# Optimization experiments

Measured on AMD Instinct MI355X. Metric: run time of the kernel, lower is better.

Reference implementation:

```python
import jax, jax.numpy as jnp
import numpy as np

VISUAL_WEIGHT = 0.01

def setup_inputs() -> dict:
    key = jax.random.key(0)
    ks = jax.random.split(key, 10)
    h = w = 96
    inp = {
        'feat_src': jax.random.normal(ks[0], (1, 256, h, w), jnp.float32),
        'feat_ref': jax.random.normal(ks[1], (1, 256, h, w), jnp.float32),
        'landmarks_src': jax.random.normal(ks[2], (1, 136, h, w), jnp.float32),
        'landmarks_ref': jax.random.normal(ks[3], (1, 136, h, w), jnp.float32),
        'mask_src': jax.random.randint(ks[4], (1, 1, h, w), 0, 3, jnp.int32),
        'mask_ref': jax.random.randint(ks[5], (1, 1, h, w), 0, 3, jnp.int32),
        'conv1_w': jax.random.normal(ks[6], (256,), jnp.float32) * 0.05,
        'conv1_b': jax.random.normal(ks[7], (1,), jnp.float32) * 0.05,
        'conv2_w': jax.random.normal(ks[8], (256,), jnp.float32) * 0.05,
        'conv2_b': jax.random.normal(ks[9], (1,), jnp.float32) * 0.05,
    }
    return inp

def reference(feat_src, feat_ref, landmarks_src, landmarks_ref, mask_src, mask_ref,
              conv1_w, conv1_b, conv2_w, conv2_b):
    b, c, h, w = feat_src.shape  # b == 1 assumed by original code
    hw = h * w
    ck = c + 136
    # 1x1 convs (256 -> 1): einsum over channel
    beta = jnp.einsum('bchw,c->bhw', feat_ref, conv1_w) + conv1_b[:, None, None]  # (1,h,w)
    gama = jnp.einsum('bchw,c->bhw', feat_ref, conv2_w) + conv2_b[:, None, None]
    # concat visual features with landmark heatmaps, then RAW reshape (as in torch)
    src = jnp.concatenate([VISUAL_WEIGHT * feat_src, landmarks_src], axis=1)  # (1,392,h,w)
    ref = jnp.concatenate([VISUAL_WEIGHT * feat_ref, landmarks_ref], axis=1)
    feat_lm_src = jnp.reshape(src, (hw, ck))   # raw reshape, faithful to torch
    feat_lm_ref = jnp.reshape(ref, (ck, hw))
    # element-wise mask equality -> (hw,) vector, broadcast over columns of A
    M = (jnp.reshape(mask_src, (hw,)) == jnp.reshape(mask_ref, (hw,))).astype(feat_src.dtype)
    A = feat_lm_src @ feat_lm_ref            # (hw, hw)
    A = jax.nn.softmax(A, axis=0)
    A = A * M                                 # broadcast on last dim, same as torch
    beta_hat = jnp.reshape(A @ jnp.reshape(beta, (hw, 1)), (1, h, w))
    gama_hat = jnp.reshape(A @ jnp.reshape(gama, (hw, 1)), (1, h, w))
    # gama_hat.expand((1,1,h,w)) * feat_src + beta_hat
    feat_src_trans = gama_hat[None] * feat_src + beta_hat[None]
    return feat_src_trans
```

## Files before the change

### kernel.cpp

```cpp
#include <hip/hip_runtime.h>

#define HW    9216
#define CK    392
#define NVIS  2359296
#define KP    672
#define NKT   21
#define NRB   144
#define MAXN  3584
#define NB_N  28
#define PSRC_BLOCKS 3024

typedef __bf16 bf16_t;
typedef __bf16 bf16x8 __attribute__((ext_vector_type(8)));
typedef __bf16 bf16x4v __attribute__((ext_vector_type(4)));
typedef unsigned short ushort8v __attribute__((ext_vector_type(8)));
typedef float  f32x4  __attribute__((ext_vector_type(4)));

typedef __attribute__((address_space(1))) void void_g;
typedef __attribute__((address_space(3))) void void_l;

static __device__ __forceinline__ void gload16(const void* g, void* l) {
  __builtin_amdgcn_global_load_lds((const void_g*)g, (void_l*)l, 16, 0, 0);
}

__global__ __launch_bounds__(256) void fused_prep(
    const float* __restrict__ feat_src, const float* __restrict__ lm_src,
    const float* __restrict__ fr, const int* __restrict__ ms,
    const int* __restrict__ mr, const float* __restrict__ w1,
    const float* __restrict__ b1, const float* __restrict__ w2,
    const float* __restrict__ b2,
    bf16_t* __restrict__ Sp, int* __restrict__ sel,
    float* __restrict__ wbs, float* __restrict__ wgs, int* __restrict__ cnt)
{
  __shared__ float r1[4][64], r2[4][64];
  __shared__ int sb[4], st[4];
  int bid = blockIdx.x, t = threadIdx.x;

  if (bid < PSRC_BLOCKS) {
    int tid = bid * 256 + t;
    int i = tid / 84, kc = tid - i * 84;
    int ko = kc * 8;
    int j0 = 0; bool lo = false, zero = false;
    if (kc < 49)       j0 = ko;
    else if (kc < 66)  j0 = ko - 136;
    else if (kc < 83) { j0 = ko - 272; lo = true; }
    else               zero = true;
    bf16x8 pk = {};
    if (!zero) {
      int idx0 = i * CK + j0;
      const float* src = (idx0 < NVIS) ? (feat_src + idx0) : (lm_src + (idx0 - NVIS));
      float sc = (idx0 < NVIS) ? 0.01f : 1.f;
      float4 v0 = *reinterpret_cast<const float4*>(src);
      float4 v1 = *reinterpret_cast<const float4*>(src + 4);
      float x[8] = {v0.x, v0.y, v0.z, v0.w, v1.x, v1.y, v1.z, v1.w};
      #pragma unroll
      for (int e = 0; e < 8; ++e) {
        float xv = sc * x[e];
        bf16_t h = (bf16_t)xv;
        pk[e] = lo ? (bf16_t)(xv - (float)h) : h;
      }
    }
    *reinterpret_cast<bf16x8*>(Sp + (long)tid * 8) = pk;
  } else {
    int b = bid - PSRC_BLOCKS;
    int qi = t & 63, cg = t >> 6, lane = t & 63, wid = t >> 6;
    int q0 = b * 64;
    float a1 = 0.f, a2 = 0.f;
    #pragma unroll 4
    for (int c = cg * 64; c < cg * 64 + 64; ++c) {
      float v = fr[(long)c * HW + q0 + qi];
      a1 += v * w1[c]; a2 += v * w2[c];
    }
    r1[cg][qi] = a1; r2[cg][qi] = a2;
    int cb = 0, ct = 0;
    for (int q = t; q < HW; q += 256) {
      bool f = (ms[q] == mr[q]);
      ct += f ? 1 : 0;
      cb += (f && q < q0) ? 1 : 0;
    }
    #pragma unroll
    for (int d = 1; d < 64; d <<= 1) {
      cb += __shfl_xor(cb, d);
      ct += __shfl_xor(ct, d);
    }
    if (lane == 0) { sb[wid] = cb; st[wid] = ct; }
    __syncthreads();
    int base = sb[0] + sb[1] + sb[2] + sb[3];
    if (t == 0 && b == 0) cnt[0] = st[0] + st[1] + st[2] + st[3];
    if (wid == 0) {
      int q = q0 + lane;
      bool flag = (ms[q] == mr[q]);
      unsigned long long mk = __ballot(flag);
      int pos = __popcll(mk & ((1ull << lane) - 1ull));
      if (flag) {
        int idx = base + pos;
        sel[idx] = q;
        wbs[idx] = r1[0][lane] + r1[1][lane] + r1[2][lane] + r1[3][lane] + b1[0];
        wgs[idx] = r2[0][lane] + r2[1][lane] + r2[2][lane] + r2[3][lane] + b2[0];
      }
    }
  }
}

__global__ __launch_bounds__(256) void prep_ref(
    const float* __restrict__ feat_ref, const float* __restrict__ lm_ref,
    const int* __restrict__ sel, const int* __restrict__ cnt,
    bf16_t* __restrict__ Rp)
{
  int nsel = cnt[0];
  int n128 = (nsel + 127) & ~127;
  int qt = blockIdx.y;
  if (qt * 32 >= n128) return;
  __shared__ bf16_t tile[32][33];
  int x = threadIdx.x & 31, y = threadIdx.x >> 5;
  int kt = blockIdx.x;
  int n = qt * 32 + x;
  int q = (n < nsel) ? sel[n] : -1;
  #pragma unroll
  for (int ry = 0; ry < 4; ++ry) {
    int kl = y + ry * 8;
    int k = kt * 32 + kl;
    int j = -1; bool lo = false;
    if (k < 392)      j = k;
    else if (k < 528) { j = k - 136; lo = true; }
    else if (k < 664) j = k - 272;
    bf16_t v = (bf16_t)0.f;
    if (j >= 0 && q >= 0) {
      int idx = j * HW + q;
      float xv = (idx < NVIS) ? 0.01f * feat_ref[idx] : lm_ref[idx - NVIS];
      bf16_t h = (bf16_t)xv;
      v = lo ? (bf16_t)(xv - (float)h) : h;
    }
    tile[kl][x] = v;
  }
  __syncthreads();
  #pragma unroll
  for (int ry = 0; ry < 4; ++ry) {
    int ql = y + ry * 8;
    int k = kt * 32 + x;
    Rp[(long)(qt * 32 + ql) * KP + k] = tile[x][ql];
  }
}

__global__ __launch_bounds__(256, 2) void gemm_e(
    const bf16_t* __restrict__ Sp, const bf16_t* __restrict__ Rp,
    const int* __restrict__ cnt, bf16_t* __restrict__ E, float* __restrict__ pd)
{
  const int bm = blockIdx.x, bn = blockIdx.y;
  if (bn * 128 >= ((cnt[0] + 127) & ~127)) return;
  __shared__ __align__(16) bf16_t As[128 * 32];
  __shared__ __align__(16) bf16_t Bs[128 * 32];
  const int t = threadIdx.x, w = t >> 6, lane = t & 63;
  const int wr = w >> 1, wc = w & 1;
  f32x4 acc[4][4] = {};

  const int chs = ((lane & 3) ^ ((lane >> 3) & 3)) * 8;
  const bf16_t* sA = Sp + (long)(bm * 128 + w * 32 + (lane >> 2)) * KP + chs;
  const bf16_t* sB = Rp + (long)(bn * 128 + w * 32 + (lane >> 2)) * KP + chs;
  bf16_t* lA = As + w * 1024;
  bf16_t* lB = Bs + w * 1024;
  const int sub = lane >> 4, r16 = lane & 15;
  const int swz = (sub ^ ((r16 >> 1) & 3)) * 8;
  const int aoff = (wr * 64 + r16) * 32 + swz;
  const int boff = (wc * 64 + r16) * 32 + swz;

  for (int kt = 0; kt < NKT; ++kt) {
    gload16(sA, lA);
    gload16(sA + 16 * KP, lA + 512);
    gload16(sB, lB);
    gload16(sB + 16 * KP, lB + 512);
    sA += 32; sB += 32;
    __syncthreads();
    bf16x8 a[4], b[4];
    #pragma unroll
    for (int m = 0; m < 4; ++m)
      a[m] = *reinterpret_cast<const bf16x8*>(As + aoff + m * 512);
    #pragma unroll
    for (int n = 0; n < 4; ++n)
      b[n] = *reinterpret_cast<const bf16x8*>(Bs + boff + n * 512);
    #pragma unroll
    for (int m = 0; m < 4; ++m)
      #pragma unroll
      for (int n = 0; n < 4; ++n)
        acc[m][n] = __builtin_amdgcn_mfma_f32_16x16x32_bf16(a[m], b[n], acc[m][n], 0, 0, 0);
    __syncthreads();
  }

  #pragma unroll
  for (int m = 0; m < 4; ++m)
    #pragma unroll
    for (int n = 0; n < 4; ++n)
      #pragma unroll
      for (int r = 0; r < 4; ++r)
        acc[m][n][r] = __expf(acc[m][n][r]);

  const int C = bn * 128 + wc * 64;
  {
    const int rb = bm * 2 + wr;
    float s[4];
    #pragma unroll
    for (int n = 0; n < 4; ++n) {
      float v = 0.f;
      #pragma unroll
      for (int m = 0; m < 4; ++m)
        #pragma unroll
        for (int r = 0; r < 4; ++r) v += acc[m][n][r];
      v += __shfl_xor(v, 16);
      v += __shfl_xor(v, 32);
      s[n] = v;
    }
    if (sub == 0) {
      f32x4 sv = {s[0], s[1], s[2], s[3]};
      *reinterpret_cast<f32x4*>(pd + (long)rb * MAXN + C + r16 * 4) = sv;
    }
  }
  bf16_t* Eb = E + (long)(bm * 128 + wr * 64 + sub * 4) * MAXN + C + r16 * 4;
  #pragma unroll
  for (int m = 0; m < 4; ++m)
    #pragma unroll
    for (int r = 0; r < 4; ++r) {
      bf16x4v pk;
      #pragma unroll
      for (int n = 0; n < 4; ++n) pk[n] = (bf16_t)acc[m][n][r];
      *reinterpret_cast<bf16x4v*>(Eb + (long)(m * 16 + r) * MAXN) = pk;
    }
}

__global__ __launch_bounds__(256) void make_u(
    const float* __restrict__ pd, const float* __restrict__ wbs,
    const float* __restrict__ wgs, const int* __restrict__ cnt,
    float* __restrict__ ub, float* __restrict__ ug)
{
  __shared__ float sD[4][64];
  int t = threadIdx.x, c = t & 63, g = t >> 6;
  int p = blockIdx.x * 64 + c;
  float D = 0.f;
  for (int rb = g * 36; rb < g * 36 + 36; ++rb)
    D += pd[(long)rb * MAXN + p];
  sD[g][c] = D;
  __syncthreads();
  if (g == 0) {
    int nsel = cnt[0];
    int n128 = (nsel + 127) & ~127;
    float Dt = sD[0][c] + sD[1][c] + sD[2][c] + sD[3][c];
    float vb = 0.f, vg = 0.f;
    if (p < n128) {
      int orig = (p & ~63) + (p & 3) * 16 + ((p >> 2) & 15);
      if (orig < nsel) {
        float inv = 1.f / Dt;
        vb = wbs[orig] * inv;
        vg = wgs[orig] * inv;
      }
    }
    ub[p] = vb;
    ug[p] = vg;
  }
}

__global__ __launch_bounds__(256) void matvec_fin(
    const bf16_t* __restrict__ E, const float* __restrict__ ub,
    const float* __restrict__ ug, const int* __restrict__ cnt,
    const float* __restrict__ fs, float* __restrict__ out)
{
  __shared__ float bhs[16], ghs[16];
  int t = threadIdx.x, lane = t & 63, wv = t >> 6;
  int n512 = ((((cnt[0] + 127) & ~127) + 511) & ~511);
  int R0 = blockIdx.x * 16;
  #pragma unroll
  for (int rr = 0; rr < 4; ++rr) {
    int r = wv * 4 + rr;
    const bf16_t* Er = E + (long)(R0 + r) * MAXN;
    float ab = 0.f, ag = 0.f;
    for (int base = 0; base < n512; base += 512) {
      int c0 = base + lane * 8;
      ushort8v e = *reinterpret_cast<const ushort8v*>(Er + c0);
      float4 u0a = *reinterpret_cast<const float4*>(ub + c0);
      float4 u0b = *reinterpret_cast<const float4*>(ub + c0 + 4);
      float4 u1a = *reinterpret_cast<const float4*>(ug + c0);
      float4 u1b = *reinterpret_cast<const float4*>(ug + c0 + 4);
      float u0[8] = {u0a.x, u0a.y, u0a.z, u0a.w, u0b.x, u0b.y, u0b.z, u0b.w};
      float u1[8] = {u1a.x, u1a.y, u1a.z, u1a.w, u1b.x, u1b.y, u1b.z, u1b.w};
      #pragma unroll
      for (int j = 0; j < 8; ++j) {
        float ev = __uint_as_float(((unsigned)e[j]) << 16);
        ab += ev * u0[j];
        ag += ev * u1[j];
      }
    }
    #pragma unroll
    for (int d = 1; d < 64; d <<= 1) {
      ab += __shfl_xor(ab, d);
      ag += __shfl_xor(ag, d);
    }
    if (lane == 0) { bhs[r] = ab; ghs[r] = ag; }
  }
  __syncthreads();
  int p = t & 15, cg = t >> 4;
  int P = R0 + p;
  float bv = bhs[p], gv = ghs[p];
  #pragma unroll 4
  for (int c = cg; c < 256; c += 16)
    out[(long)c * HW + P] = gv * fs[(long)c * HW + P] + bv;
}

extern "C" void kernel_launch(void* const* d_in, const int* in_sizes, int n_in,
                              void* d_out, int out_size, void* d_ws, size_t ws_size,
                              hipStream_t stream) {
  const float* feat_src = (const float*)d_in[0];
  const float* feat_ref = (const float*)d_in[1];
  const float* lm_src   = (const float*)d_in[2];
  const float* lm_ref   = (const float*)d_in[3];
  const int*   mask_src = (const int*)d_in[4];
  const int*   mask_ref = (const int*)d_in[5];
  const float* w1 = (const float*)d_in[6];
  const float* b1 = (const float*)d_in[7];
  const float* w2 = (const float*)d_in[8];
  const float* b2 = (const float*)d_in[9];
  float* out = (float*)d_out;

  char* ws = (char*)d_ws;
  bf16_t* Sp   = (bf16_t*)(ws);
  bf16_t* Rp   = (bf16_t*)(ws + 12386304);
  bf16_t* E    = (bf16_t*)(ws + 17203200);
  float* pd    = (float*)(ws + 83263488);
  float* wb    = (float*)(ws + 85327872);
  float* wg    = (float*)(ws + 85342208);
  float* ub    = (float*)(ws + 85356544);
  float* ug    = (float*)(ws + 85370880);
  int*   sel   = (int*)  (ws + 85385216);
  int*   cnt   = (int*)  (ws + 85399552);

  fused_prep<<<PSRC_BLOCKS + HW / 64, 256, 0, stream>>>(
      feat_src, lm_src, feat_ref, mask_src, mask_ref, w1, b1, w2, b2,
      Sp, sel, wb, wg, cnt);
  prep_ref<<<dim3(NKT, MAXN / 32), 256, 0, stream>>>(feat_ref, lm_ref, sel, cnt, Rp);
  gemm_e<<<dim3(72, NB_N), 256, 0, stream>>>(Sp, Rp, cnt, E, pd);
  make_u<<<MAXN / 64, 256, 0, stream>>>(pd, wb, wg, cnt, ub, ug);
  matvec_fin<<<HW / 16, 256, 0, stream>>>(E, ub, ug, cnt, feat_src, out);
}
```

Before: 183.9 us.

## Fuse ref-packing into prep kernel with per-block mask prefix scan; tighten matvec

Removes the separate prep_ref launch by having each ref-tile block recompute the mask prefix scan itself and build its own list of selected columns, so it no longer has to wait on a sel array written by another kernel. This saves one launch and one dependency, but every one of the 2352 blocks now re-reads the whole mask. matvec_fin now processes four rows per wave in one pass and stops at n128 instead of n512, which cuts redundant ub/ug loads and skips padded columns.

```diff
diff --git a/kernel.cpp b/kernel.cpp
--- a/kernel.cpp
+++ b/kernel.cpp
@@ -8,6 +8,8 @@
 #define NRB   144
 #define MAXN  3584
 #define NB_N  28
+#define PREF_BLOCKS 2352
+#define PCOL_BLOCKS 144
 #define PSRC_BLOCKS 3024
 
 typedef __bf16 bf16_t;
@@ -25,19 +27,118 @@
 
 __global__ __launch_bounds__(256) void fused_prep(
     const float* __restrict__ feat_src, const float* __restrict__ lm_src,
-    const float* __restrict__ fr, const int* __restrict__ ms,
-    const int* __restrict__ mr, const float* __restrict__ w1,
-    const float* __restrict__ b1, const float* __restrict__ w2,
-    const float* __restrict__ b2,
-    bf16_t* __restrict__ Sp, int* __restrict__ sel,
+    const float* __restrict__ fr, const float* __restrict__ lm_ref,
+    const int* __restrict__ ms, const int* __restrict__ mr,
+    const float* __restrict__ w1, const float* __restrict__ b1,
+    const float* __restrict__ w2, const float* __restrict__ b2,
+    bf16_t* __restrict__ Sp, bf16_t* __restrict__ Rp,
     float* __restrict__ wbs, float* __restrict__ wgs, int* __restrict__ cnt)
 {
   __shared__ float r1[4][64], r2[4][64];
   __shared__ int sb[4], st[4];
+  __shared__ int qlist[32];
+  __shared__ bf16_t tile[32][33];
   int bid = blockIdx.x, t = threadIdx.x;
-
-  if (bid < PSRC_BLOCKS) {
-    int tid = bid * 256 + t;
+  int lane = t & 63, wid = t >> 6;
+
+  if (bid < PREF_BLOCKS) {
+    int qt = bid / NKT, kt = bid - qt * NKT;
+    int n0 = qt * 32;
+    if (t < 32) qlist[t] = -1;
+    int c = 0;
+    #pragma unroll
+    for (int i = 0; i < 36; ++i) {
+      int q = t * 36 + i;
+      c += (ms[q] == mr[q]) ? 1 : 0;
+    }
+    int pref = c;
+    #pragma unroll
+    for (int d = 1; d < 64; d <<= 1) {
+      int v = __shfl_up(pref, d);
+      if (lane >= d) pref += v;
+    }
+    if (lane == 63) { sb[wid] = pref; }
+    __syncthreads();
+    int wbase = 0;
+    for (int wv = 0; wv < wid; ++wv) wbase += sb[wv];
+    int rank = wbase + pref - c;
+    int nsel = sb[0] + sb[1] + sb[2] + sb[3];
+    int n128 = (nsel + 127) & ~127;
+    #pragma unroll
+    for (int i = 0; i < 36; ++i) {
+      int q = t * 36 + i;
+      if (ms[q] == mr[q]) {
+        if (rank >= n0 && rank < n0 + 32) qlist[rank - n0] = q;
+        ++rank;
+      }
+    }
+    __syncthreads();
+    if (n0 >= n128) return;
+    int x = t & 31, y = t >> 5;
+    int q = qlist[x];
+    #pragma unroll
+    for (int ry = 0; ry < 4; ++ry) {
+      int kl = y + ry * 8;
+      int k = kt * 32 + kl;
+      int j = -1; bool lo = false;
+      if (k < 392)      j = k;
+      else if (k < 528) { j = k - 136; lo = true; }
+      else if (k < 664) j = k - 272;
+      bf16_t v = (bf16_t)0.f;
+      if (j >= 0 && q >= 0) {
+        int idx = j * HW + q;
+        float xv = (idx < NVIS) ? 0.01f * fr[idx] : lm_ref[idx - NVIS];
+        bf16_t h = (bf16_t)xv;
+        v = lo ? (bf16_t)(xv - (float)h) : h;
+      }
+      tile[kl][x] = v;
+    }
+    __syncthreads();
+    #pragma unroll
+    for (int ry = 0; ry < 4; ++ry) {
+      int ql = y + ry * 8;
+      int k = kt * 32 + x;
+      Rp[(long)(n0 + ql) * KP + k] = tile[x][ql];
+    }
+  } else if (bid < PREF_BLOCKS + PCOL_BLOCKS) {
+    int b = bid - PREF_BLOCKS;
+    int qi = t & 63, cg = t >> 6;
+    int q0 = b * 64;
+    float a1 = 0.f, a2 = 0.f;
+    #pragma unroll 4
+    for (int c = cg * 64; c < cg * 64 + 64; ++c) {
+      float v = fr[(long)c * HW + q0 + qi];
+      a1 += v * w1[c]; a2 += v * w2[c];
+    }
+    r1[cg][qi] = a1; r2[cg][qi] = a2;
+    int cb = 0, ct = 0;
+    for (int q = t; q < HW; q += 256) {
+      bool f = (ms[q] == mr[q]);
+      ct += f ? 1 : 0;
+      cb += (f && q < q0) ? 1 : 0;
+    }
+    #pragma unroll
+    for (int d = 1; d < 64; d <<= 1) {
+      cb += __shfl_xor(cb, d);
+      ct += __shfl_xor(ct, d);
+    }
+    if (lane == 0) { sb[wid] = cb; st[wid] = ct; }
+    __syncthreads();
+    int base = sb[0] + sb[1] + sb[2] + sb[3];
+    if (t == 0 && b == 0) cnt[0] = st[0] + st[1] + st[2] + st[3];
+    if (wid == 0) {
+      int q = q0 + lane;
+      bool flag = (ms[q] == mr[q]);
+      unsigned long long mk = __ballot(flag);
+      int pos = __popcll(mk & ((1ull << lane) - 1ull));
+      if (flag) {
+        int idx = base + pos;
+        wbs[idx] = r1[0][lane] + r1[1][lane] + r1[2][lane] + r1[3][lane] + b1[0];
+        wgs[idx] = r2[0][lane] + r2[1][lane] + r2[2][lane] + r2[3][lane] + b2[0];
+      }
+    }
+  } else {
+    int tid = (bid - PREF_BLOCKS - PCOL_BLOCKS) * 256 + t;
     int i = tid / 84, kc = tid - i * 84;
     int ko = kc * 8;
     int j0 = 0; bool lo = false, zero = false;
@@ -61,84 +162,6 @@
       }
     }
     *reinterpret_cast<bf16x8*>(Sp + (long)tid * 8) = pk;
-  } else {
-    int b = bid - PSRC_BLOCKS;
-    int qi = t & 63, cg = t >> 6, lane = t & 63, wid = t >> 6;
-    int q0 = b * 64;
-    float a1 = 0.f, a2 = 0.f;
-    #pragma unroll 4
-    for (int c = cg * 64; c < cg * 64 + 64; ++c) {
-      float v = fr[(long)c * HW + q0 + qi];
-      a1 += v * w1[c]; a2 += v * w2[c];
-    }
-    r1[cg][qi] = a1; r2[cg][qi] = a2;
-    int cb = 0, ct = 0;
-    for (int q = t; q < HW; q += 256) {
-      bool f = (ms[q] == mr[q]);
-      ct += f ? 1 : 0;
-      cb += (f && q < q0) ? 1 : 0;
-    }
-    #pragma unroll
-    for (int d = 1; d < 64; d <<= 1) {
-      cb += __shfl_xor(cb, d);
-      ct += __shfl_xor(ct, d);
-    }
-    if (lane == 0) { sb[wid] = cb; st[wid] = ct; }
-    __syncthreads();
-    int base = sb[0] + sb[1] + sb[2] + sb[3];
-    if (t == 0 && b == 0) cnt[0] = st[0] + st[1] + st[2] + st[3];
-    if (wid == 0) {
-      int q = q0 + lane;
-      bool flag = (ms[q] == mr[q]);
-      unsigned long long mk = __ballot(flag);
-      int pos = __popcll(mk & ((1ull << lane) - 1ull));
-      if (flag) {
-        int idx = base + pos;
-        sel[idx] = q;
-        wbs[idx] = r1[0][lane] + r1[1][lane] + r1[2][lane] + r1[3][lane] + b1[0];
-        wgs[idx] = r2[0][lane] + r2[1][lane] + r2[2][lane] + r2[3][lane] + b2[0];
-      }
-    }
-  }
-}
-
-__global__ __launch_bounds__(256) void prep_ref(
-    const float* __restrict__ feat_ref, const float* __restrict__ lm_ref,
-    const int* __restrict__ sel, const int* __restrict__ cnt,
-    bf16_t* __restrict__ Rp)
-{
-  int nsel = cnt[0];
-  int n128 = (nsel + 127) & ~127;
-  int qt = blockIdx.y;
-  if (qt * 32 >= n128) return;
-  __shared__ bf16_t tile[32][33];
-  int x = threadIdx.x & 31, y = threadIdx.x >> 5;
-  int kt = blockIdx.x;
-  int n = qt * 32 + x;
-  int q = (n < nsel) ? sel[n] : -1;
-  #pragma unroll
-  for (int ry = 0; ry < 4; ++ry) {
-    int kl = y + ry * 8;
-    int k = kt * 32 + kl;
-    int j = -1; bool lo = false;
-    if (k < 392)      j = k;
-    else if (k < 528) { j = k - 136; lo = true; }
-    else if (k < 664) j = k - 272;
-    bf16_t v = (bf16_t)0.f;
-    if (j >= 0 && q >= 0) {
-      int idx = j * HW + q;
-      float xv = (idx < NVIS) ? 0.01f * feat_ref[idx] : lm_ref[idx - NVIS];
-      bf16_t h = (bf16_t)xv;
-      v = lo ? (bf16_t)(xv - (float)h) : h;
-    }
-    tile[kl][x] = v;
-  }
-  __syncthreads();
-  #pragma unroll
-  for (int ry = 0; ry < 4; ++ry) {
-    int ql = y + ry * 8;
-    int k = kt * 32 + x;
-    Rp[(long)(qt * 32 + ql) * KP + k] = tile[x][ql];
   }
 }
 
@@ -264,16 +287,13 @@
 {
   __shared__ float bhs[16], ghs[16];
   int t = threadIdx.x, lane = t & 63, wv = t >> 6;
-  int n512 = ((((cnt[0] + 127) & ~127) + 511) & ~511);
+  int n128 = (cnt[0] + 127) & ~127;
   int R0 = blockIdx.x * 16;
-  #pragma unroll
-  for (int rr = 0; rr < 4; ++rr) {
-    int r = wv * 4 + rr;
-    const bf16_t* Er = E + (long)(R0 + r) * MAXN;
-    float ab = 0.f, ag = 0.f;
-    for (int base = 0; base < n512; base += 512) {
-      int c0 = base + lane * 8;
-      ushort8v e = *reinterpret_cast<const ushort8v*>(Er + c0);
+  const bf16_t* Ew = E + (long)(R0 + wv * 4) * MAXN;
+  float ab[4] = {}, ag[4] = {};
+  for (int base = 0; base < n128; base += 512) {
+    int c0 = base + lane * 8;
+    if (c0 < n128) {
       float4 u0a = *reinterpret_cast<const float4*>(ub + c0);
       float4 u0b = *reinterpret_cast<const float4*>(ub + c0 + 4);
       float4 u1a = *reinterpret_cast<const float4*>(ug + c0);
@@ -281,18 +301,25 @@
       float u0[8] = {u0a.x, u0a.y, u0a.z, u0a.w, u0b.x, u0b.y, u0b.z, u0b.w};
       float u1[8] = {u1a.x, u1a.y, u1a.z, u1a.w, u1b.x, u1b.y, u1b.z, u1b.w};
       #pragma unroll
-      for (int j = 0; j < 8; ++j) {
-        float ev = __uint_as_float(((unsigned)e[j]) << 16);
-        ab += ev * u0[j];
-        ag += ev * u1[j];
-      }
-    }
+      for (int rr = 0; rr < 4; ++rr) {
+        ushort8v e = *reinterpret_cast<const ushort8v*>(Ew + (long)rr * MAXN + c0);
+        #pragma unroll
+        for (int j = 0; j < 8; ++j) {
+          float ev = __uint_as_float(((unsigned)e[j]) << 16);
+          ab[rr] += ev * u0[j];
+          ag[rr] += ev * u1[j];
+        }
+      }
+    }
+  }
+  #pragma unroll
+  for (int rr = 0; rr < 4; ++rr) {
     #pragma unroll
     for (int d = 1; d < 64; d <<= 1) {
-      ab += __shfl_xor(ab, d);
-      ag += __shfl_xor(ag, d);
-    }
-    if (lane == 0) { bhs[r] = ab; ghs[r] = ag; }
+      ab[rr] += __shfl_xor(ab[rr], d);
+      ag[rr] += __shfl_xor(ag[rr], d);
+    }
+    if (lane == 0) { bhs[wv * 4 + rr] = ab[rr]; ghs[wv * 4 + rr] = ag[rr]; }
   }
   __syncthreads();
   int p = t & 15, cg = t >> 4;
@@ -327,13 +354,11 @@
   float* wg    = (float*)(ws + 85342208);
   float* ub    = (float*)(ws + 85356544);
   float* ug    = (float*)(ws + 85370880);
-  int*   sel   = (int*)  (ws + 85385216);
-  int*   cnt   = (int*)  (ws + 85399552);
-
-  fused_prep<<<PSRC_BLOCKS + HW / 64, 256, 0, stream>>>(
-      feat_src, lm_src, feat_ref, mask_src, mask_ref, w1, b1, w2, b2,
-      Sp, sel, wb, wg, cnt);
-  prep_ref<<<dim3(NKT, MAXN / 32), 256, 0, stream>>>(feat_ref, lm_ref, sel, cnt, Rp);
+  int*   cnt   = (int*)  (ws + 85385216);
+
+  fused_prep<<<PREF_BLOCKS + PCOL_BLOCKS + PSRC_BLOCKS, 256, 0, stream>>>(
+      feat_src, lm_src, feat_ref, lm_ref, mask_src, mask_ref, w1, b1, w2, b2,
+      Sp, Rp, wb, wg, cnt);
   gemm_e<<<dim3(72, NB_N), 256, 0, stream>>>(Sp, Rp, cnt, E, pd);
   make_u<<<MAXN / 64, 256, 0, stream>>>(pd, wb, wg, cnt, ub, ug);
   matvec_fin<<<HW / 16, 256, 0, stream>>>(E, ub, ug, cnt, feat_src, out);
```

After: 300.3 us. +63.2%, slower.
